# Kernel optimization log

Measured on AMD Instinct MI355X. Metric: run time of the kernel, lower is better.

## Reference

```python
import jax, jax.numpy as jnp
import numpy as np

B, S, H = 2, 2048, 2048
NH, NKV, HD = 16, 4, 128
ROPE_BASE = 10000.0


def hbit_linear(x, w):
    # BitNet: 8-bit per-token absmax activation quant, ternary (2-bit) weight quant
    s = 127.0 / jnp.clip(jnp.max(jnp.abs(x), axis=-1, keepdims=True), 1e-5, None)
    xq = jnp.clip(jnp.round(x * s), -128, 127) / s
    ws = 1.0 / jnp.clip(jnp.mean(jnp.abs(w)), 1e-5, None)
    wq = jnp.clip(jnp.round(w * ws), -1, 1) / ws
    return xq @ wq.T


def rotate_half(x):
    h = x.shape[-1] // 2
    return jnp.concatenate([-x[..., h:], x[..., :h]], axis=-1)


def rope_cos_sin(position_ids, head_dim, dtype):
    inv_freq = 1.0 / (ROPE_BASE ** (jnp.arange(0, head_dim, 2, dtype=jnp.float32) / head_dim))
    freqs = position_ids.astype(jnp.float32)[..., None] * inv_freq[None, None, :]  # (b,s,hd/2)
    emb = jnp.concatenate([freqs, freqs], axis=-1)  # (b,s,hd)
    return jnp.cos(emb).astype(dtype)[:, :, None, :], jnp.sin(emb).astype(dtype)[:, :, None, :]


def setup_inputs() -> dict:
    key = jax.random.key(0)
    ks = jax.random.split(key, 5)
    xavier = lambda k, shp: jax.random.uniform(k, shp, jnp.float32, -1.0, 1.0) * np.sqrt(6.0 / (shp[0] + shp[1]))
    causal = jnp.where(jnp.tril(jnp.ones((S, S), bool)), 0.0, -1e9).astype(jnp.float32)[None, None]
    return {
        "hidden_states": jax.random.normal(ks[0], (B, S, H), jnp.float32),
        "attention_mask": causal,
        "Wq": xavier(ks[1], (H, H)),
        "Wk": xavier(ks[2], (NKV * HD, H)),
        "Wv": xavier(ks[3], (NKV * HD, H)),
        "Wo": xavier(ks[4], (H, H)),
        "position_ids": jnp.arange(S, dtype=jnp.int64 if jax.config.jax_enable_x64 else jnp.int32)[None, :],
    }


def reference(hidden_states, attention_mask, Wq, Wk, Wv, Wo, position_ids):
    b, s, _ = hidden_states.shape
    q = hbit_linear(hidden_states, Wq).reshape(b, s, NH, HD)
    k = hbit_linear(hidden_states, Wk).reshape(b, s, NKV, HD)
    v = hbit_linear(hidden_states, Wv).reshape(b, s, NKV, HD)
    cos, sin = rope_cos_sin(position_ids, HD, q.dtype)  # (1,s,1,hd)
    q = q * cos + rotate_half(q) * sin
    k = k * cos + rotate_half(k) * sin
    n_rep = NH // NKV
    k = jnp.repeat(k, n_rep, axis=2)  # (b,s,NH,hd)
    v = jnp.repeat(v, n_rep, axis=2)
    scale = 1.0 / np.sqrt(HD)
    scores = jnp.einsum("bqhd,bkhd->bhqk", q, k) * scale + attention_mask
    probs = jax.nn.softmax(scores, axis=-1)  # dropout inactive (eval)
    out = jnp.einsum("bhqk,bkhd->bqhd", probs, v).reshape(b, s, NH * HD)
    return hbit_linear(out, Wo)
```

## Files before the change

kernel.cpp:

```cpp
#include <hip/hip_runtime.h>
#include <hip/hip_bf16.h>

#define B_ 2
#define S_ 2048
#define H_ 2048
#define NH_ 16
#define NKV_ 4
#define HD_ 128
#define M_ (B_*S_)
#define KVD_ (NKV_*HD_)

typedef signed char s8;
typedef __attribute__((ext_vector_type(8))) short short8;
typedef __attribute__((ext_vector_type(4))) float f32x4;
typedef __attribute__((ext_vector_type(4))) int int4v;

__device__ __forceinline__ float loadf(const void* p, long i, int isb){
  if (isb) return __bfloat162float(((const __hip_bfloat16*)p)[i]);
  return ((const float*)p)[i];
}

__device__ __forceinline__ unsigned short f2bf(float f){
  union { float f; unsigned u; } v; v.f = f;
  unsigned r = v.u + 0x7FFF + ((v.u >> 16) & 1);
  return (unsigned short)(r >> 16);
}

__device__ __forceinline__ float bf2f(unsigned short b){
  union { unsigned u; float f; } v; v.u = ((unsigned)b) << 16; return v.f;
}

__device__ __forceinline__ void gl2lds16(const void* g, void* l){
  __builtin_amdgcn_global_load_lds(
      (const __attribute__((address_space(1))) void*)g,
      (__attribute__((address_space(3))) void*)l, 16, 0, 0);
}

__global__ void k_detect(const unsigned int* x, int* flag){
  __shared__ int sh[256];
  int t = threadIdx.x, c = 0;
  for (int i = t; i < 2048; i += 256){
    unsigned e = (x[i] >> 7) & 0xFF;
    if (e >= 90 && e <= 150) c++;
  }
  sh[t] = c; __syncthreads();
  for (int k = 128; k > 0; k >>= 1){ if (t < k) sh[t] += sh[t+k]; __syncthreads(); }
  if (t == 0) flag[0] = (sh[0] > 1228) ? 1 : 0;
}

__global__ void k_prep(const void* Wq, const void* Wk, const void* Wv, const void* Wo,
                       const int* flag, float* wsum, float* ct, float* st){
  int bid = blockIdx.x, t = threadIdx.x;
  if (t < 64){
    float inv = exp2f(-(float)t * 0.20762050593045952f);
    float a = (float)bid * inv;
    float sn, cs; sincosf(a, &sn, &cs);
    ct[bid*64 + t] = cs; st[bid*64 + t] = sn;
  }
  __shared__ float sh[256];
  int isb = *flag;
  const void* w; long n; int wi; long b0; int nb;
  if (bid < 768)       { w = Wq; wi = 0; n = (long)H_*H_;   b0 = bid;      nb = 768; }
  else if (bid < 1024) { w = Wk; wi = 1; n = (long)KVD_*H_; b0 = bid-768;  nb = 256; }
  else if (bid < 1280) { w = Wv; wi = 2; n = (long)KVD_*H_; b0 = bid-1024; nb = 256; }
  else                 { w = Wo; wi = 3; n = (long)H_*H_;   b0 = bid-1280; nb = 768; }
  float s = 0.f;
  for (long i = b0*256 + t; i < n; i += (long)nb*256) s += fabsf(loadf(w, i, isb));
  sh[t] = s; __syncthreads();
  for (int k = 128; k > 0; k >>= 1){ if (t < k) sh[t] += sh[t+k]; __syncthreads(); }
  if (t == 0) atomicAdd(&wsum[wi], sh[0]);
}

__global__ void k_wquant_all(const void* Wq, const void* Wk, const void* Wv, const void* Wo,
                             const int* flag, const float* wsum,
                             s8* oq, s8* ok, s8* ov, s8* oo){
  int isb = *flag;
  int bid = blockIdx.x, t = threadIdx.x;
  const float cntq = (float)((long)H_*H_), cntkv = (float)((long)KVD_*H_);
  const void* w; s8* out; long n; int wi; long b0; int nb; float cnt;
  if (bid < 1024)      { w = Wq; out = oq; wi = 0; n = (long)H_*H_;   b0 = bid;       nb = 1024; cnt = cntq; }
  else if (bid < 1280) { w = Wk; out = ok; wi = 1; n = (long)KVD_*H_; b0 = bid-1024;  nb = 256;  cnt = cntkv; }
  else if (bid < 1536) { w = Wv; out = ov; wi = 2; n = (long)KVD_*H_; b0 = bid-1280;  nb = 256;  cnt = cntkv; }
  else                 { w = Wo; out = oo; wi = 3; n = (long)H_*H_;   b0 = bid-1536;  nb = 1024; cnt = cntq; }
  float mean = fmaxf(wsum[wi] / cnt, 1e-5f);
  float sc = 1.0f / mean;
  for (long i = b0*256 + t; i < n; i += (long)nb*256){
    float v = rintf(loadf(w, i, isb) * sc);
    v = fminf(fmaxf(v, -1.f), 1.f);
    out[i] = (s8)v;
  }
}

__global__ void k_aquant_in(const void* x, const int* flag, float* srow, s8* xq){
  __shared__ float sh[256];
  int isb = *flag; int r = blockIdx.x, t = threadIdx.x;
  long base = (long)r * H_;
  float v[8];
  if (isb){
    uint4 wv = ((const uint4*)((const unsigned short*)x + base))[t];
    unsigned u[4] = {wv.x, wv.y, wv.z, wv.w};
    #pragma unroll
    for (int i = 0; i < 4; i++){
      v[2*i]   = bf2f((unsigned short)(u[i] & 0xFFFF));
      v[2*i+1] = bf2f((unsigned short)(u[i] >> 16));
    }
  } else {
    const float4* p = (const float4*)((const float*)x + base);
    float4 a = p[t*2], b2 = p[t*2+1];
    v[0]=a.x; v[1]=a.y; v[2]=a.z; v[3]=a.w; v[4]=b2.x; v[5]=b2.y; v[6]=b2.z; v[7]=b2.w;
  }
  float mx = 0.f;
  #pragma unroll
  for (int i = 0; i < 8; i++) mx = fmaxf(mx, fabsf(v[i]));
  sh[t] = mx; __syncthreads();
  for (int k = 128; k > 0; k >>= 1){ if (t < k) sh[t] = fmaxf(sh[t], sh[t+k]); __syncthreads(); }
  float s = 127.0f / fmaxf(sh[0], 1e-5f);
  if (t == 0) srow[r] = s;
  unsigned long long pk = 0;
  #pragma unroll
  for (int i = 0; i < 8; i++){
    float q = fminf(fmaxf(rintf(v[i] * s), -128.f), 127.f);
    pk |= ((unsigned long long)(unsigned char)(s8)q) << (8*i);
  }
  *(unsigned long long*)(xq + base + t*8) = pk;
}

__global__ void k_aquant_bf16(const unsigned short* __restrict__ x, float* __restrict__ srow, s8* __restrict__ xq){
  __shared__ float sh[256];
  int r = blockIdx.x, t = threadIdx.x;
  long base = (long)r * H_;
  uint4 wv = ((const uint4*)(x + base))[t];
  unsigned u[4] = {wv.x, wv.y, wv.z, wv.w};
  float v[8];
  #pragma unroll
  for (int i = 0; i < 4; i++){
    v[2*i]   = bf2f((unsigned short)(u[i] & 0xFFFF));
    v[2*i+1] = bf2f((unsigned short)(u[i] >> 16));
  }
  float mx = 0.f;
  #pragma unroll
  for (int i = 0; i < 8; i++) mx = fmaxf(mx, fabsf(v[i]));
  sh[t] = mx; __syncthreads();
  for (int k = 128; k > 0; k >>= 1){ if (t < k) sh[t] = fmaxf(sh[t], sh[t+k]); __syncthreads(); }
  float s = 127.0f / fmaxf(sh[0], 1e-5f);
  if (t == 0) srow[r] = s;
  unsigned long long pk = 0;
  #pragma unroll
  for (int i = 0; i < 8; i++){
    float q = fminf(fmaxf(rintf(v[i] * s), -128.f), 127.f);
    pk |= ((unsigned long long)(unsigned char)(s8)q) << (8*i);
  }
  *(unsigned long long*)(xq + base + t*8) = pk;
}

__device__ __forceinline__ void gemm_core(
      const s8* __restrict__ A, const s8* __restrict__ Bw, s8* As, s8* Bs,
      const float* __restrict__ srow, float mean,
      void* __restrict__ Cout, int N, int mode, int isb,
      unsigned short* __restrict__ Vt,
      const float* __restrict__ ct, const float* __restrict__ st, long bcol){
  int tid = threadIdx.x;
  int wave = tid >> 6, lane = tid & 63;
  int quad = lane >> 4, c = lane & 15;
  int wm = wave >> 1, wn = wave & 1;
  long arow = (long)blockIdx.y * 128;
  const int K = H_;

  int4v acc[4][4];
  #pragma unroll
  for (int mt = 0; mt < 4; mt++)
    #pragma unroll
    for (int nt = 0; nt < 4; nt++) acc[mt][nt] = (int4v){0,0,0,0};

  int rl = lane >> 2;
  int kq = (lane & 3) ^ ((lane >> 3) & 3);
  int ch0 = wave*2, ch1 = wave*2 + 1;
  long gA0 = (arow + ch0*16 + rl)*(long)K + kq*16;
  long gA1 = (arow + ch1*16 + rl)*(long)K + kq*16;
  long gB0 = (bcol + ch0*16 + rl)*(long)K + kq*16;
  long gB1 = (bcol + ch1*16 + rl)*(long)K + kq*16;

  int sA = quad ^ ((c >> 1) & 3);
  int ntl[4];
  #pragma unroll
  for (int nt = 0; nt < 4; nt++) ntl[nt] = 2*wn + (nt & 1) + 4*(nt >> 1);
  int frA[4], frB[4];
  #pragma unroll
  for (int mt = 0; mt < 4; mt++) frA[mt] = (wm*64 + mt*16 + c)*64 + sA*16;
  #pragma unroll
  for (int nt = 0; nt < 4; nt++) frB[nt] = (ntl[nt]*16 + c)*64 + sA*16;

  for (int k0 = 0; k0 < K; k0 += 64){
    gl2lds16(A  + gA0 + k0, As + ch0*1024);
    gl2lds16(A  + gA1 + k0, As + ch1*1024);
    gl2lds16(Bw + gB0 + k0, Bs + ch0*1024);
    gl2lds16(Bw + gB1 + k0, Bs + ch1*1024);
    __syncthreads();
    int4v afr[4], bfr[4];
    #pragma unroll
    for (int mt = 0; mt < 4; mt++) afr[mt] = *(const int4v*)&As[frA[mt]];
    #pragma unroll
    for (int nt = 0; nt < 4; nt++) bfr[nt] = *(const int4v*)&Bs[frB[nt]];
    #pragma unroll
    for (int mt = 0; mt < 4; mt++)
      #pragma unroll
      for (int nt = 0; nt < 4; nt++)
        acc[mt][nt] = __builtin_amdgcn_mfma_i32_16x16x64_i8(afr[mt], bfr[nt], acc[mt][nt], 0, 0, 0);
    __syncthreads();
  }

  if (mode == 0 || mode == 3){
    unsigned short* Ob = (unsigned short*)Cout;
    #pragma unroll
    for (int mt = 0; mt < 4; mt++){
      #pragma unroll
      for (int r = 0; r < 4; r++){
        long grow = arow + wm*64 + mt*16 + quad*4 + r;
        float sc = mean / srow[grow];
        if (mode == 0) sc *= 0.12751743f;
        int pos = (int)(grow & (S_-1));
        #pragma unroll
        for (int p = 0; p < 2; p++){
          int col_lo = (int)bcol + (2*wn + p)*16 + c;
          int d = col_lo & 63;
          float cv = ct[pos*64 + d], sv = st[pos*64 + d];
          float vlo = acc[mt][p][r]   * sc;
          float vhi = acc[mt][p+2][r] * sc;
          Ob[grow*(long)N + col_lo]      = f2bf(vlo*cv - vhi*sv);
          Ob[grow*(long)N + col_lo + 64] = f2bf(vhi*cv + vlo*sv);
        }
      }
    }
  } else if (mode == 1){
    #pragma unroll
    for (int mt = 0; mt < 4; mt++){
      #pragma unroll
      for (int r = 0; r < 4; r++){
        long grow = arow + wm*64 + mt*16 + quad*4 + r;
        float sc = mean / srow[grow];
        long bb = grow >> 11; int sI = (int)(grow & (S_-1));
        unsigned short* base = Vt + bb*(long)KVD_*S_ + sI;
        #pragma unroll
        for (int nt = 0; nt < 4; nt++)
          base[(long)(bcol + ntl[nt]*16 + c)*S_] = f2bf(acc[mt][nt][r] * sc);
      }
    }
  } else {
    #pragma unroll
    for (int mt = 0; mt < 4; mt++){
      #pragma unroll
      for (int r = 0; r < 4; r++){
        long grow = arow + wm*64 + mt*16 + quad*4 + r;
        float sc = mean / srow[grow];
        long cb = grow*(long)N + bcol + c;
        if (isb){
          __hip_bfloat16* o = (__hip_bfloat16*)Cout;
          #pragma unroll
          for (int nt = 0; nt < 4; nt++)
            o[cb + ntl[nt]*16] = __float2bfloat16(acc[mt][nt][r] * sc);
        } else {
          float* o = (float*)Cout;
          #pragma unroll
          for (int nt = 0; nt < 4; nt++)
            o[cb + ntl[nt]*16] = acc[mt][nt][r] * sc;
        }
      }
    }
  }
}

__global__ __launch_bounds__(256, 2) void k_gemm_qkv(
      const s8* __restrict__ xq,
      const s8* __restrict__ wqq, const s8* __restrict__ wkq, const s8* __restrict__ wvq,
      const float* __restrict__ srow, const float* __restrict__ wsum,
      unsigned short* __restrict__ Qb, unsigned short* __restrict__ Kb,
      unsigned short* __restrict__ Vt,
      const float* __restrict__ ct, const float* __restrict__ st){
  __shared__ __align__(16) s8 As[128*64];
  __shared__ __align__(16) s8 Bs[128*64];
  int bx = blockIdx.x;
  const float cntq = (float)((long)H_*H_), cntkv = (float)((long)KVD_*H_);
  const s8* Bw; void* Cout; unsigned short* vt = nullptr;
  int N, mode; float mean; long bcol;
  if (bx < 16){
    Bw = wqq; Cout = Qb; N = H_;   mode = 0; mean = fmaxf(wsum[0]/cntq, 1e-5f);  bcol = (long)bx*128;
  } else if (bx < 20){
    Bw = wkq; Cout = Kb; N = KVD_; mode = 3; mean = fmaxf(wsum[1]/cntkv, 1e-5f); bcol = (long)(bx-16)*128;
  } else {
    Bw = wvq; Cout = nullptr; vt = Vt; N = KVD_; mode = 1; mean = fmaxf(wsum[2]/cntkv, 1e-5f); bcol = (long)(bx-20)*128;
  }
  gemm_core(xq, Bw, As, Bs, srow, mean, Cout, N, mode, 0, vt, ct, st, bcol);
}

__global__ __launch_bounds__(256, 2) void k_gemm_o(
      const s8* __restrict__ aq, const s8* __restrict__ woq,
      const float* __restrict__ srow, const float* __restrict__ wsum,
      const int* __restrict__ flag, void* __restrict__ out,
      const float* __restrict__ ct, const float* __restrict__ st){
  __shared__ __align__(16) s8 As[128*64];
  __shared__ __align__(16) s8 Bs[128*64];
  float mean = fmaxf(wsum[3] / (float)((long)H_*H_), 1e-5f);
  gemm_core(aq, woq, As, Bs, srow, mean, out, H_, 2, *flag, nullptr, ct, st, (long)blockIdx.x*128);
}

#define PSTR 40
__global__ __launch_bounds__(256) void k_attn_mfma(const unsigned short* __restrict__ Qb,
    const unsigned short* __restrict__ Kb, const unsigned short* __restrict__ Vt,
    unsigned short* __restrict__ ob){
  int wid = threadIdx.x >> 6, lane = threadIdx.x & 63;
  int quad = lane >> 4, c = lane & 15;
  int kvh = blockIdx.y, b = blockIdx.z;
  int win = blockIdx.x;
  if (b == 1) win = (S_/32 - 1) - win;
  int h = kvh*4 + wid;
  int q0 = win*32;

  __shared__ __align__(16) unsigned short Ks[2][64*128];
  __shared__ __align__(16) unsigned short Vs[128*64];
  __shared__ __align__(16) unsigned short Ps[4][16*PSTR];

  short8 qf[2][4];
  #pragma unroll
  for (int t0 = 0; t0 < 2; t0++)
    #pragma unroll
    for (int f = 0; f < 4; f++)
      qf[t0][f] = *(const short8*)(Qb + ((long)(b*S_ + q0 + t0*16 + c)*NH_ + h)*HD_ + f*32 + quad*8);

  const unsigned short* Kg = Kb + (long)b*S_*KVD_ + kvh*HD_;
  const unsigned short* Vg = Vt + ((long)b*KVD_ + kvh*HD_)*S_;

  f32x4 o[2][8], ol[2];
  #pragma unroll
  for (int t0 = 0; t0 < 2; t0++){
    #pragma unroll
    for (int i = 0; i < 8; i++) o[t0][i] = (f32x4){0.f,0.f,0.f,0.f};
    ol[t0] = (f32x4){0.f,0.f,0.f,0.f};
  }
  short8 ones;
  #pragma unroll
  for (int i = 0; i < 8; i++) ones[i] = (short)0x3F80;

  int skey = lane >> 4;
  int kslot = lane & 15;
  int vrow = lane >> 3;
  int vslot = lane & 7;

  int nk = q0 + 32;
  #pragma unroll
  for (int i = 0; i < 4; i++){
    int kk = wid*16 + i*4;
    int key = kk + skey;
    int g = kslot ^ (key & 15);
    gl2lds16(Kg + (long)key*KVD_ + g*8, &Ks[0][kk*128]);
  }

  int buf = 0;
  for (int kc = 0; kc < nk; kc += 64, buf ^= 1){
    __syncthreads();
    #pragma unroll
    for (int i = 0; i < 4; i++){
      int rr = wid*32 + i*8;
      int hd = rr + vrow;
      int g = vslot ^ (hd & 7);
      gl2lds16(Vg + (long)hd*S_ + kc + g*8, &Vs[rr*64]);
    }

    f32x4 s[2][4];
    #pragma unroll
    for (int t0 = 0; t0 < 2; t0++)
      #pragma unroll
      for (int kt = 0; kt < 4; kt++) s[t0][kt] = (f32x4){0.f,0.f,0.f,0.f};
    #pragma unroll
    for (int kt = 0; kt < 4; kt++){
      short8 kf4[4];
      #pragma unroll
      for (int f = 0; f < 4; f++)
        kf4[f] = *(const short8*)&Ks[buf][(kt*16 + c)*128 + ((f*4 + quad) ^ c)*8];
      #pragma unroll
      for (int t0 = 0; t0 < 2; t0++)
        #pragma unroll
        for (int f = 0; f < 4; f++)
          s[t0][kt] = __builtin_amdgcn_mfma_f32_16x16x32_bf16(kf4[f], qf[t0][f], s[t0][kt], 0, 0, 0);
    }
    #pragma unroll
    for (int t0 = 0; t0 < 2; t0++){
      int qv = q0 + t0*16 + c;
      if (kc + 63 > q0 + t0*16){
        #pragma unroll
        for (int kt = 0; kt < 4; kt++){
          #pragma unroll
          for (int r = 0; r < 4; r++){
            int key = kc + kt*16 + quad*4 + r;
            if (key > qv) s[t0][kt][r] = -1e30f;
          }
        }
      }
    }

    __syncthreads();

    if (kc + 64 < nk){
      #pragma unroll
      for (int i = 0; i < 4; i++){
        int kk = wid*16 + i*4;
        int key = kk + skey;
        int g = kslot ^ (key & 15);
        gl2lds16(Kg + (long)(kc + 64 + key)*KVD_ + g*8, &Ks[buf^1][kk*128]);
      }
    }

    #pragma unroll
    for (int pp = 0; pp < 2; pp++){
      short8 vf[8];
      #pragma unroll
      for (int nt = 0; nt < 8; nt++)
        vf[nt] = *(const short8*)&Vs[(nt*16 + c)*64 + ((pp*4 + quad) ^ (c & 7))*8];
      #pragma unroll
      for (int t0 = 0; t0 < 2; t0++){
        #pragma unroll
        for (int tk = 0; tk < 2; tk++){
          f32x4 sv = s[t0][pp*2 + tk];
          float e0 = exp2f(sv[0]), e1 = exp2f(sv[1]);
          float e2 = exp2f(sv[2]), e3 = exp2f(sv[3]);
          unsigned w0, w1;
          asm("v_cvt_pk_bf16_f32 %0, %1, %2" : "=v"(w0) : "v"(e0), "v"(e1));
          asm("v_cvt_pk_bf16_f32 %0, %1, %2" : "=v"(w1) : "v"(e2), "v"(e3));
          uint2 pkv; pkv.x = w0; pkv.y = w1;
          *(uint2*)&Ps[wid][c*PSTR + tk*16 + quad*4] = pkv;
        }
        short8 pf = *(const short8*)&Ps[wid][c*PSTR + quad*8];
        #pragma unroll
        for (int nt = 0; nt < 8; nt++)
          o[t0][nt] = __builtin_amdgcn_mfma_f32_16x16x32_bf16(pf, vf[nt], o[t0][nt], 0, 0, 0);
        ol[t0] = __builtin_amdgcn_mfma_f32_16x16x32_bf16(pf, ones, ol[t0], 0, 0, 0);
      }
    }
  }

  #pragma unroll
  for (int t0 = 0; t0 < 2; t0++){
    float il[4];
    #pragma unroll
    for (int r = 0; r < 4; r++) il[r] = 1.0f / ol[t0][r];
    #pragma unroll
    for (int nt = 0; nt < 8; nt++)
      #pragma unroll
      for (int r = 0; r < 4; r++)
        ob[((long)(b*S_ + q0 + t0*16 + quad*4 + r))*H_ + h*HD_ + nt*16 + c] = f2bf(o[t0][nt][r]*il[r]);
  }
}

extern "C" void kernel_launch(void* const* d_in, const int* in_sizes, int n_in,
                              void* d_out, int out_size, void* d_ws, size_t ws_size,
                              hipStream_t stream){
  (void)in_sizes; (void)n_in; (void)out_size; (void)ws_size;
  const void* x  = d_in[0];
  const void* Wq = d_in[2];
  const void* Wk = d_in[3];
  const void* Wv = d_in[4];
  const void* Wo = d_in[5];
  char* ws = (char*)d_ws;
  size_t o = 0;
  auto alloc = [&](size_t b){ size_t r = o; o += (b + 255) & ~(size_t)255; return r; };
  size_t META = alloc(256);
  float* wsum = (float*)(ws + META);
  int*   flag = (int*)  (ws + META + 32);
  float* s_x = (float*)(ws + alloc((size_t)M_*4));
  float* s_a = (float*)(ws + alloc((size_t)M_*4));
  float* ct  = (float*)(ws + alloc((size_t)S_*64*4));
  float* st  = (float*)(ws + alloc((size_t)S_*64*4));
  s8* xq  = (s8*)(ws + alloc((size_t)M_*H_));
  s8* wqq = (s8*)(ws + alloc((size_t)H_*H_));
  s8* wkq = (s8*)(ws + alloc((size_t)KVD_*H_));
  s8* wvq = (s8*)(ws + alloc((size_t)KVD_*H_));
  s8* woq = (s8*)(ws + alloc((size_t)H_*H_));
  unsigned short* Qb = (unsigned short*)(ws + alloc((size_t)M_*NH_*HD_*2));
  unsigned short* Kb = (unsigned short*)(ws + alloc((size_t)M_*KVD_*2));
  unsigned short* Vt = (unsigned short*)(ws + alloc((size_t)M_*KVD_*2));
  unsigned short* ab = (unsigned short*)(ws + alloc((size_t)M_*H_*2));
  s8* aq = xq;

  hipMemsetAsync(ws + META, 0, 64, stream);
  k_detect<<<1,256,0,stream>>>((const unsigned int*)x, flag);
  k_prep<<<2048,256,0,stream>>>(Wq, Wk, Wv, Wo, flag, wsum, ct, st);
  k_wquant_all<<<2560,256,0,stream>>>(Wq, Wk, Wv, Wo, flag, wsum, wqq, wkq, wvq, woq);
  k_aquant_in<<<M_,256,0,stream>>>(x, flag, s_x, xq);

  dim3 gqkv(16+4+4, M_/128);
  k_gemm_qkv<<<gqkv, 256, 0, stream>>>(xq, wqq, wkq, wvq, s_x, wsum, Qb, Kb, Vt, ct, st);

  dim3 ga(S_/32, NKV_, B_);
  k_attn_mfma<<<ga, 256, 0, stream>>>(Qb, Kb, Vt, ab);

  k_aquant_bf16<<<M_,256,0,stream>>>(ab, s_a, aq);

  dim3 go(H_/128, M_/128);
  k_gemm_o<<<go, 256, 0, stream>>>(aq, woq, s_a, wsum, flag, d_out, ct, st);
}
```

Measured before the change: 313.8 us.

## Split attention KV range across two blocks and merge partials in activation quant

The attention kernel now launches twice as many blocks when workspace allows. Each block handles alternating 64-key chunks of the causal range and writes a normalized partial output plus its row-sum. The activation-quant kernel merges the two partials, weighting each by its row-sum, before quantizing. K double-buffering is dropped to a single buffer and launch bounds request 4 blocks per SM, aiming for more parallelism and occupancy. The cost is extra partial-output traffic and less load/compute overlap. It also relies on the existing no-max softmax, so both partials share the same exponent scale.

```diff
diff --git a/kernel.cpp b/kernel.cpp
--- a/kernel.cpp
+++ b/kernel.cpp
@@ -125,17 +125,34 @@
   *(unsigned long long*)(xq + base + t*8) = pk;
 }
 
-__global__ void k_aquant_bf16(const unsigned short* __restrict__ x, float* __restrict__ srow, s8* __restrict__ xq){
+__global__ void k_aquant_bf16(const unsigned short* __restrict__ x0,
+                              const unsigned short* __restrict__ x1,
+                              const float* __restrict__ lp0, const float* __restrict__ lp1,
+                              float* __restrict__ srow, s8* __restrict__ xq){
   __shared__ float sh[256];
   int r = blockIdx.x, t = threadIdx.x;
   long base = (long)r * H_;
-  uint4 wv = ((const uint4*)(x + base))[t];
-  unsigned u[4] = {wv.x, wv.y, wv.z, wv.w};
   float v[8];
-  #pragma unroll
-  for (int i = 0; i < 4; i++){
-    v[2*i]   = bf2f((unsigned short)(u[i] & 0xFFFF));
-    v[2*i+1] = bf2f((unsigned short)(u[i] >> 16));
+  uint4 a0 = ((const uint4*)(x0 + base))[t];
+  unsigned u0[4] = {a0.x, a0.y, a0.z, a0.w};
+  if (lp1){
+    int h = t >> 4;
+    float l0 = lp0[(long)r*NH_ + h], l1 = lp1[(long)r*NH_ + h];
+    float inv = 1.0f / (l0 + l1);
+    float w0 = l0 * inv, w1 = l1 * inv;
+    uint4 a1 = ((const uint4*)(x1 + base))[t];
+    unsigned u1[4] = {a1.x, a1.y, a1.z, a1.w};
+    #pragma unroll
+    for (int i = 0; i < 4; i++){
+      v[2*i]   = bf2f((unsigned short)(u0[i] & 0xFFFF))*w0 + bf2f((unsigned short)(u1[i] & 0xFFFF))*w1;
+      v[2*i+1] = bf2f((unsigned short)(u0[i] >> 16))*w0   + bf2f((unsigned short)(u1[i] >> 16))*w1;
+    }
+  } else {
+    #pragma unroll
+    for (int i = 0; i < 4; i++){
+      v[2*i]   = bf2f((unsigned short)(u0[i] & 0xFFFF));
+      v[2*i+1] = bf2f((unsigned short)(u0[i] >> 16));
+    }
   }
   float mx = 0.f;
   #pragma unroll
@@ -304,20 +321,28 @@
 }
 
 #define PSTR 40
-__global__ __launch_bounds__(256) void k_attn_mfma(const unsigned short* __restrict__ Qb,
+__global__ __launch_bounds__(256, 4) void k_attn_mfma(const unsigned short* __restrict__ Qb,
     const unsigned short* __restrict__ Kb, const unsigned short* __restrict__ Vt,
-    unsigned short* __restrict__ ob){
+    unsigned short* __restrict__ on0, unsigned short* __restrict__ on1,
+    float* __restrict__ lp0, float* __restrict__ lp1, int nsplit){
   int wid = threadIdx.x >> 6, lane = threadIdx.x & 63;
   int quad = lane >> 4, c = lane & 15;
   int kvh = blockIdx.y, b = blockIdx.z;
-  int win = blockIdx.x;
+  int bx = blockIdx.x;
+  int win, sp;
+  if (nsplit == 2){ win = bx >> 1; sp = bx & 1; }
+  else            { win = bx;      sp = 0;      }
   if (b == 1) win = (S_/32 - 1) - win;
   int h = kvh*4 + wid;
   int q0 = win*32;
-
-  __shared__ __align__(16) unsigned short Ks[2][64*128];
+  int kstep = nsplit*64;
+
+  __shared__ __align__(16) unsigned short Ks[64*128];
   __shared__ __align__(16) unsigned short Vs[128*64];
   __shared__ __align__(16) unsigned short Ps[4][16*PSTR];
+
+  unsigned short* on = sp ? on1 : on0;
+  float*          lp = sp ? lp1 : lp0;
 
   short8 qf[2][4];
   #pragma unroll
@@ -346,93 +371,96 @@
   int vslot = lane & 7;
 
   int nk = q0 + 32;
-  #pragma unroll
-  for (int i = 0; i < 4; i++){
-    int kk = wid*16 + i*4;
-    int key = kk + skey;
-    int g = kslot ^ (key & 15);
-    gl2lds16(Kg + (long)key*KVD_ + g*8, &Ks[0][kk*128]);
-  }
-
-  int buf = 0;
-  for (int kc = 0; kc < nk; kc += 64, buf ^= 1){
-    __syncthreads();
+  int kc0 = sp * 64;
+
+  if (kc0 < nk){
     #pragma unroll
     for (int i = 0; i < 4; i++){
-      int rr = wid*32 + i*8;
-      int hd = rr + vrow;
-      int g = vslot ^ (hd & 7);
-      gl2lds16(Vg + (long)hd*S_ + kc + g*8, &Vs[rr*64]);
-    }
-
-    f32x4 s[2][4];
-    #pragma unroll
-    for (int t0 = 0; t0 < 2; t0++)
-      #pragma unroll
-      for (int kt = 0; kt < 4; kt++) s[t0][kt] = (f32x4){0.f,0.f,0.f,0.f};
-    #pragma unroll
-    for (int kt = 0; kt < 4; kt++){
-      short8 kf4[4];
-      #pragma unroll
-      for (int f = 0; f < 4; f++)
-        kf4[f] = *(const short8*)&Ks[buf][(kt*16 + c)*128 + ((f*4 + quad) ^ c)*8];
+      int kk = wid*16 + i*4;
+      int key = kk + skey;
+      int g = kslot ^ (key & 15);
+      gl2lds16(Kg + (long)(kc0 + key)*KVD_ + g*8, &Ks[kk*128]);
+    }
+
+    for (int kc = kc0; kc < nk; kc += kstep){
+      __syncthreads();
+      #pragma unroll
+      for (int i = 0; i < 4; i++){
+        int rr = wid*32 + i*8;
+        int hd = rr + vrow;
+        int g = vslot ^ (hd & 7);
+        gl2lds16(Vg + (long)hd*S_ + kc + g*8, &Vs[rr*64]);
+      }
+
+      f32x4 s[2][4];
       #pragma unroll
       for (int t0 = 0; t0 < 2; t0++)
         #pragma unroll
+        for (int kt = 0; kt < 4; kt++) s[t0][kt] = (f32x4){0.f,0.f,0.f,0.f};
+      #pragma unroll
+      for (int kt = 0; kt < 4; kt++){
+        short8 kf4[4];
+        #pragma unroll
         for (int f = 0; f < 4; f++)
-          s[t0][kt] = __builtin_amdgcn_mfma_f32_16x16x32_bf16(kf4[f], qf[t0][f], s[t0][kt], 0, 0, 0);
-    }
-    #pragma unroll
-    for (int t0 = 0; t0 < 2; t0++){
-      int qv = q0 + t0*16 + c;
-      if (kc + 63 > q0 + t0*16){
-        #pragma unroll
-        for (int kt = 0; kt < 4; kt++){
+          kf4[f] = *(const short8*)&Ks[(kt*16 + c)*128 + ((f*4 + quad) ^ c)*8];
+        #pragma unroll
+        for (int t0 = 0; t0 < 2; t0++)
           #pragma unroll
-          for (int r = 0; r < 4; r++){
-            int key = kc + kt*16 + quad*4 + r;
-            if (key > qv) s[t0][kt][r] = -1e30f;
+          for (int f = 0; f < 4; f++)
+            s[t0][kt] = __builtin_amdgcn_mfma_f32_16x16x32_bf16(kf4[f], qf[t0][f], s[t0][kt], 0, 0, 0);
+      }
+      #pragma unroll
+      for (int t0 = 0; t0 < 2; t0++){
+        int qv = q0 + t0*16 + c;
+        if (kc + 63 > q0 + t0*16){
+          #pragma unroll
+          for (int kt = 0; kt < 4; kt++){
+            #pragma unroll
+            for (int r = 0; r < 4; r++){
+              int key = kc + kt*16 + quad*4 + r;
+              if (key > qv) s[t0][kt][r] = -1e30f;
+            }
           }
         }
       }
-    }
-
-    __syncthreads();
-
-    if (kc + 64 < nk){
-      #pragma unroll
-      for (int i = 0; i < 4; i++){
-        int kk = wid*16 + i*4;
-        int key = kk + skey;
-        int g = kslot ^ (key & 15);
-        gl2lds16(Kg + (long)(kc + 64 + key)*KVD_ + g*8, &Ks[buf^1][kk*128]);
-      }
-    }
-
-    #pragma unroll
-    for (int pp = 0; pp < 2; pp++){
-      short8 vf[8];
-      #pragma unroll
-      for (int nt = 0; nt < 8; nt++)
-        vf[nt] = *(const short8*)&Vs[(nt*16 + c)*64 + ((pp*4 + quad) ^ (c & 7))*8];
-      #pragma unroll
-      for (int t0 = 0; t0 < 2; t0++){
-        #pragma unroll
-        for (int tk = 0; tk < 2; tk++){
-          f32x4 sv = s[t0][pp*2 + tk];
-          float e0 = exp2f(sv[0]), e1 = exp2f(sv[1]);
-          float e2 = exp2f(sv[2]), e3 = exp2f(sv[3]);
-          unsigned w0, w1;
-          asm("v_cvt_pk_bf16_f32 %0, %1, %2" : "=v"(w0) : "v"(e0), "v"(e1));
-          asm("v_cvt_pk_bf16_f32 %0, %1, %2" : "=v"(w1) : "v"(e2), "v"(e3));
-          uint2 pkv; pkv.x = w0; pkv.y = w1;
-          *(uint2*)&Ps[wid][c*PSTR + tk*16 + quad*4] = pkv;
+
+      __syncthreads();
+
+      if (kc + kstep < nk){
+        #pragma unroll
+        for (int i = 0; i < 4; i++){
+          int kk = wid*16 + i*4;
+          int key = kk + skey;
+          int g = kslot ^ (key & 15);
+          gl2lds16(Kg + (long)(kc + kstep + key)*KVD_ + g*8, &Ks[kk*128]);
         }
-        short8 pf = *(const short8*)&Ps[wid][c*PSTR + quad*8];
+      }
+
+      #pragma unroll
+      for (int pp = 0; pp < 2; pp++){
+        short8 vf[8];
         #pragma unroll
         for (int nt = 0; nt < 8; nt++)
-          o[t0][nt] = __builtin_amdgcn_mfma_f32_16x16x32_bf16(pf, vf[nt], o[t0][nt], 0, 0, 0);
-        ol[t0] = __builtin_amdgcn_mfma_f32_16x16x32_bf16(pf, ones, ol[t0], 0, 0, 0);
+          vf[nt] = *(const short8*)&Vs[(nt*16 + c)*64 + ((pp*4 + quad) ^ (c & 7))*8];
+        #pragma unroll
+        for (int t0 = 0; t0 < 2; t0++){
+          #pragma unroll
+          for (int tk = 0; tk < 2; tk++){
+            f32x4 sv = s[t0][pp*2 + tk];
+            float e0 = exp2f(sv[0]), e1 = exp2f(sv[1]);
+            float e2 = exp2f(sv[2]), e3 = exp2f(sv[3]);
+            unsigned w0, w1;
+            asm("v_cvt_pk_bf16_f32 %0, %1, %2" : "=v"(w0) : "v"(e0), "v"(e1));
+            asm("v_cvt_pk_bf16_f32 %0, %1, %2" : "=v"(w1) : "v"(e2), "v"(e3));
+            uint2 pkv; pkv.x = w0; pkv.y = w1;
+            *(uint2*)&Ps[wid][c*PSTR + tk*16 + quad*4] = pkv;
+          }
+          short8 pf = *(const short8*)&Ps[wid][c*PSTR + quad*8];
+          #pragma unroll
+          for (int nt = 0; nt < 8; nt++)
+            o[t0][nt] = __builtin_amdgcn_mfma_f32_16x16x32_bf16(pf, vf[nt], o[t0][nt], 0, 0, 0);
+          ol[t0] = __builtin_amdgcn_mfma_f32_16x16x32_bf16(pf, ones, ol[t0], 0, 0, 0);
+        }
       }
     }
   }
@@ -441,19 +469,22 @@
   for (int t0 = 0; t0 < 2; t0++){
     float il[4];
     #pragma unroll
-    for (int r = 0; r < 4; r++) il[r] = 1.0f / ol[t0][r];
-    #pragma unroll
-    for (int nt = 0; nt < 8; nt++)
-      #pragma unroll
-      for (int r = 0; r < 4; r++)
-        ob[((long)(b*S_ + q0 + t0*16 + quad*4 + r))*H_ + h*HD_ + nt*16 + c] = f2bf(o[t0][nt][r]*il[r]);
+    for (int r = 0; r < 4; r++) il[r] = ol[t0][r] > 0.f ? 1.0f / ol[t0][r] : 0.f;
+    #pragma unroll
+    for (int r = 0; r < 4; r++){
+      long row = (long)(b*S_ + q0 + t0*16 + quad*4 + r);
+      lp[row*NH_ + h] = ol[t0][r];
+      #pragma unroll
+      for (int nt = 0; nt < 8; nt++)
+        on[row*H_ + h*HD_ + nt*16 + c] = f2bf(o[t0][nt][r]*il[r]);
+    }
   }
 }
 
 extern "C" void kernel_launch(void* const* d_in, const int* in_sizes, int n_in,
                               void* d_out, int out_size, void* d_ws, size_t ws_size,
                               hipStream_t stream){
-  (void)in_sizes; (void)n_in; (void)out_size; (void)ws_size;
+  (void)in_sizes; (void)n_in; (void)out_size;
   const void* x  = d_in[0];
   const void* Wq = d_in[2];
   const void* Wk = d_in[3];
@@ -477,8 +508,20 @@
   unsigned short* Qb = (unsigned short*)(ws + alloc((size_t)M_*NH_*HD_*2));
   unsigned short* Kb = (unsigned short*)(ws + alloc((size_t)M_*KVD_*2));
   unsigned short* Vt = (unsigned short*)(ws + alloc((size_t)M_*KVD_*2));
-  unsigned short* ab = (unsigned short*)(ws + alloc((size_t)M_*H_*2));
+  unsigned short* ab0 = (unsigned short*)(ws + alloc((size_t)M_*H_*2));
+  float* lp0 = (float*)(ws + alloc((size_t)M_*NH_*4));
   s8* aq = xq;
+
+  size_t need1 = ((size_t)M_*H_*2 + 255) & ~(size_t)255;
+  size_t need2 = ((size_t)M_*NH_*4 + 255) & ~(size_t)255;
+  int nsplit = 1;
+  unsigned short* ab1 = nullptr;
+  float* lp1 = nullptr;
+  if (ws_size >= o + need1 + need2){
+    ab1 = (unsigned short*)(ws + alloc((size_t)M_*H_*2));
+    lp1 = (float*)(ws + alloc((size_t)M_*NH_*4));
+    nsplit = 2;
+  }
 
   hipMemsetAsync(ws + META, 0, 64, stream);
   k_detect<<<1,256,0,stream>>>((const unsigned int*)x, flag);
@@ -489,10 +532,10 @@
   dim3 gqkv(16+4+4, M_/128);
   k_gemm_qkv<<<gqkv, 256, 0, stream>>>(xq, wqq, wkq, wvq, s_x, wsum, Qb, Kb, Vt, ct, st);
 
-  dim3 ga(S_/32, NKV_, B_);
-  k_attn_mfma<<<ga, 256, 0, stream>>>(Qb, Kb, Vt, ab);
-
-  k_aquant_bf16<<<M_,256,0,stream>>>(ab, s_a, aq);
+  dim3 ga(S_/32*nsplit, NKV_, B_);
+  k_attn_mfma<<<ga, 256, 0, stream>>>(Qb, Kb, Vt, ab0, ab1, lp0, lp1, nsplit);
+
+  k_aquant_bf16<<<M_,256,0,stream>>>(ab0, ab1, lp0, lp1, s_a, aq);
 
   dim3 go(H_/128, M_/128);
   k_gemm_o<<<go, 256, 0, stream>>>(aq, woq, s_a, wsum, flag, d_out, ct, st);
```

Result: slower. 505.9 us (+61.2%).

## Remap GEMM and attention blocks per XCD and single-buffer attention K tile

Applied to the files above, without the earlier changes.

Replaces the 2D/3D grids of the QKV GEMM, output GEMM and attention kernels with 1D grids. Each linear block id is decoded so that blocks landing on the same XCD (id mod 8) share the same row panels or the same batch/KV-head, which is meant to improve L2 reuse of the A operand and of K/V. The attention kernel also drops K double buffering in LDS to cut shared memory, which may allow more resident blocks but exposes K load latency. The new attention order walks windows from short to long and loses the old reversal that balanced the causal work, so the heaviest blocks now run last and may leave a tail.

```diff
diff --git a/kernel.cpp b/kernel.cpp
--- a/kernel.cpp
+++ b/kernel.cpp
@@ -158,12 +158,12 @@
       const float* __restrict__ srow, float mean,
       void* __restrict__ Cout, int N, int mode, int isb,
       unsigned short* __restrict__ Vt,
-      const float* __restrict__ ct, const float* __restrict__ st, long bcol){
+      const float* __restrict__ ct, const float* __restrict__ st,
+      long bcol, long arow){
   int tid = threadIdx.x;
   int wave = tid >> 6, lane = tid & 63;
   int quad = lane >> 4, c = lane & 15;
   int wm = wave >> 1, wn = wave & 1;
-  long arow = (long)blockIdx.y * 128;
   const int K = H_;
 
   int4v acc[4][4];
@@ -278,7 +278,11 @@
       const float* __restrict__ ct, const float* __restrict__ st){
   __shared__ __align__(16) s8 As[128*64];
   __shared__ __align__(16) s8 Bs[128*64];
-  int bx = blockIdx.x;
+  int lid = blockIdx.x;
+  int xcd = lid & 7;
+  int rem = lid >> 3;
+  int by  = xcd*4 + (rem & 3);
+  int bx  = rem >> 2;
   const float cntq = (float)((long)H_*H_), cntkv = (float)((long)KVD_*H_);
   const s8* Bw; void* Cout; unsigned short* vt = nullptr;
   int N, mode; float mean; long bcol;
@@ -289,7 +293,7 @@
   } else {
     Bw = wvq; Cout = nullptr; vt = Vt; N = KVD_; mode = 1; mean = fmaxf(wsum[2]/cntkv, 1e-5f); bcol = (long)(bx-20)*128;
   }
-  gemm_core(xq, Bw, As, Bs, srow, mean, Cout, N, mode, 0, vt, ct, st, bcol);
+  gemm_core(xq, Bw, As, Bs, srow, mean, Cout, N, mode, 0, vt, ct, st, bcol, (long)by*128);
 }
 
 __global__ __launch_bounds__(256, 2) void k_gemm_o(
@@ -299,8 +303,14 @@
       const float* __restrict__ ct, const float* __restrict__ st){
   __shared__ __align__(16) s8 As[128*64];
   __shared__ __align__(16) s8 Bs[128*64];
+  int lid = blockIdx.x;
+  int xcd = lid & 7;
+  int rem = lid >> 3;
+  int by  = xcd*4 + (rem & 3);
+  int bx  = rem >> 2;
   float mean = fmaxf(wsum[3] / (float)((long)H_*H_), 1e-5f);
-  gemm_core(aq, woq, As, Bs, srow, mean, out, H_, 2, *flag, nullptr, ct, st, (long)blockIdx.x*128);
+  gemm_core(aq, woq, As, Bs, srow, mean, out, H_, 2, *flag, nullptr, ct, st,
+            (long)bx*128, (long)by*128);
 }
 
 #define PSTR 40
@@ -309,13 +319,14 @@
     unsigned short* __restrict__ ob){
   int wid = threadIdx.x >> 6, lane = threadIdx.x & 63;
   int quad = lane >> 4, c = lane & 15;
-  int kvh = blockIdx.y, b = blockIdx.z;
-  int win = blockIdx.x;
-  if (b == 1) win = (S_/32 - 1) - win;
+  int lid = blockIdx.x;
+  int panel = lid & 7;
+  int kvh = panel & 3, b = panel >> 2;
+  int win = lid >> 3;
   int h = kvh*4 + wid;
   int q0 = win*32;
 
-  __shared__ __align__(16) unsigned short Ks[2][64*128];
+  __shared__ __align__(16) unsigned short Ks[64*128];
   __shared__ __align__(16) unsigned short Vs[128*64];
   __shared__ __align__(16) unsigned short Ps[4][16*PSTR];
 
@@ -351,11 +362,10 @@
     int kk = wid*16 + i*4;
     int key = kk + skey;
     int g = kslot ^ (key & 15);
-    gl2lds16(Kg + (long)key*KVD_ + g*8, &Ks[0][kk*128]);
-  }
-
-  int buf = 0;
-  for (int kc = 0; kc < nk; kc += 64, buf ^= 1){
+    gl2lds16(Kg + (long)key*KVD_ + g*8, &Ks[kk*128]);
+  }
+
+  for (int kc = 0; kc < nk; kc += 64){
     __syncthreads();
     #pragma unroll
     for (int i = 0; i < 4; i++){
@@ -375,7 +385,7 @@
       short8 kf4[4];
       #pragma unroll
       for (int f = 0; f < 4; f++)
-        kf4[f] = *(const short8*)&Ks[buf][(kt*16 + c)*128 + ((f*4 + quad) ^ c)*8];
+        kf4[f] = *(const short8*)&Ks[(kt*16 + c)*128 + ((f*4 + quad) ^ c)*8];
       #pragma unroll
       for (int t0 = 0; t0 < 2; t0++)
         #pragma unroll
@@ -405,7 +415,7 @@
         int kk = wid*16 + i*4;
         int key = kk + skey;
         int g = kslot ^ (key & 15);
-        gl2lds16(Kg + (long)(kc + 64 + key)*KVD_ + g*8, &Ks[buf^1][kk*128]);
+        gl2lds16(Kg + (long)(kc + 64 + key)*KVD_ + g*8, &Ks[kk*128]);
       }
     }
 
@@ -486,14 +496,11 @@
   k_wquant_all<<<2560,256,0,stream>>>(Wq, Wk, Wv, Wo, flag, wsum, wqq, wkq, wvq, woq);
   k_aquant_in<<<M_,256,0,stream>>>(x, flag, s_x, xq);
 
-  dim3 gqkv(16+4+4, M_/128);
-  k_gemm_qkv<<<gqkv, 256, 0, stream>>>(xq, wqq, wkq, wvq, s_x, wsum, Qb, Kb, Vt, ct, st);
-
-  dim3 ga(S_/32, NKV_, B_);
-  k_attn_mfma<<<ga, 256, 0, stream>>>(Qb, Kb, Vt, ab);
+  k_gemm_qkv<<<768, 256, 0, stream>>>(xq, wqq, wkq, wvq, s_x, wsum, Qb, Kb, Vt, ct, st);
+
+  k_attn_mfma<<<512, 256, 0, stream>>>(Qb, Kb, Vt, ab);
 
   k_aquant_bf16<<<M_,256,0,stream>>>(ab, s_a, aq);
 
-  dim3 go(H_/128, M_/128);
-  k_gemm_o<<<go, 256, 0, stream>>>(aq, woq, s_a, wsum, flag, d_out, ct, st);
-}
+  k_gemm_o<<<512, 256, 0, stream>>>(aq, woq, s_a, wsum, flag, d_out, ct, st);
+}
```

Result: no change. 318.4 us (+1.5%).
